# Kernel tuning notes

Measured on AMD Instinct MI355X. Metric: run time of the kernel, lower is better.

## Reference

```python
import jax, jax.numpy as jnp
import numpy as np

B, S, D, H = 2, 2048, 1024, 16
HD = D // H  # head dim = 64


def setup_inputs() -> dict:
    key0 = jax.random.key(0)
    ks = jax.random.split(key0, 12)
    scale = 1.0 / np.sqrt(D)
    inp = {
        "query": jax.random.normal(ks[0], (B, S, D), jnp.float32),
        "key": jax.random.normal(ks[1], (B, S, D), jnp.float32),
        "value": jax.random.normal(ks[2], (B, S, D), jnp.float32),
        "mask": jax.random.randint(ks[3], (B, S), 0, 2, jnp.int32),
        "Wq": jax.random.normal(ks[4], (D, D), jnp.float32) * scale,
        "bq": jnp.zeros((D,), jnp.float32),
        "Wk": jax.random.normal(ks[5], (D, D), jnp.float32) * scale,
        "bk": jnp.zeros((D,), jnp.float32),
        "Wv": jax.random.normal(ks[6], (D, D), jnp.float32) * scale,
        "bv": jnp.zeros((D,), jnp.float32),
        "Wo": jax.random.normal(ks[7], (D, D), jnp.float32) * scale,
        "bo": jnp.zeros((D,), jnp.float32),
    }
    return inp


def _split_heads(x):  # (B,S,D) -> (B,H,S,HD)
    Bb, Ss, Dd = x.shape
    return x.reshape(Bb, Ss, H, HD).transpose(0, 2, 1, 3)


def reference(query, key, value, mask, Wq, bq, Wk, bk, Wv, bv, Wo, bo):
    # Linear projections (torch Linear: x @ W.T + b), split into heads.
    q = _split_heads(query @ Wq.T + bq)
    k = _split_heads(key @ Wk.T + bk)
    v = _split_heads(value @ Wv.T + bv)
    # Scaled dot-product scores: (B,H,S,S); NOTE: original divides by sqrt(head_dim).
    scores = jnp.einsum("bhqd,bhkd->bhqk", q, k) / np.sqrt(HD).astype(np.float32)
    # mask (B,S) masks KEY positions; broadcast over heads and query positions.
    scores = jnp.where(mask[:, None, None, :] == 0, jnp.float32(-1e9), scores)
    attn = jax.nn.softmax(scores, axis=-1)
    # Dropout is identity in eval mode.
    x = jnp.einsum("bhqk,bhkd->bhqd", attn, v)  # (B,H,S,HD)
    x = x.transpose(0, 2, 1, 3).reshape(query.shape[0], query.shape[1], D)
    return x @ Wo.T + bo
```

## Files before the change

### kernel.cpp

```cpp
#include <hip/hip_runtime.h>
#include <hip/hip_bf16.h>
#include <hip/hip_fp16.h>

#define BB 2
#define SS 2048
#define DD 1024
#define HH 16
#define HD 64
#define MM (BB * SS)

typedef __attribute__((ext_vector_type(8))) _Float16 half8;
typedef __attribute__((ext_vector_type(4))) float f32x4;
typedef __attribute__((ext_vector_type(4))) short short4v;

static __device__ __forceinline__ short f2h(float f) {
    _Float16 h = (_Float16)f;
    return __builtin_bit_cast(short, h);
}

static __device__ __forceinline__ unsigned pk2(float a, float b) {
    auto h = __builtin_amdgcn_cvt_pkrtz(a, b);
    return __builtin_bit_cast(unsigned, h);
}

static __device__ __forceinline__ float fexp2(float x) {
    return __builtin_amdgcn_exp2f(x);
}

static __device__ __forceinline__ void gload16(const void* g, void* l) {
    __builtin_amdgcn_global_load_lds(
        (const __attribute__((address_space(1))) unsigned*)g,
        (__attribute__((address_space(3))) unsigned*)l, 16, 0, 0);
}

#define SC2E 0.18033688011112042f

__global__ __launch_bounds__(256) void cvt_kernel(
    const float* __restrict__ wq, const float* __restrict__ wk,
    const float* __restrict__ wv, const float* __restrict__ wo,
    const int* __restrict__ mask,
    short* __restrict__ wq16, short* __restrict__ wk16,
    short* __restrict__ wv16, short* __restrict__ wo16,
    short* __restrict__ mask16)
{
    const int i = (blockIdx.x * 256 + threadIdx.x) * 4;
    if (blockIdx.y == 4) {
        if (i >= BB * SS) return;
        const int4 mi = *(const int4*)&mask[i];
        short4v f;
        f.x = f2h(mi.x ? 1.0f : 0.0f);
        f.y = f2h(mi.y ? 1.0f : 0.0f);
        f.z = f2h(mi.z ? 1.0f : 0.0f);
        f.w = f2h(mi.w ? 1.0f : 0.0f);
        *(short4v*)&mask16[i] = f;
        return;
    }
    const float* src; short* dst;
    switch (blockIdx.y) {
        case 0: src = wq; dst = wq16; break;
        case 1: src = wk; dst = wk16; break;
        case 2: src = wv; dst = wv16; break;
        default: src = wo; dst = wo16; break;
    }
    if (i >= DD * DD) return;
    const float4 f = *(const float4*)&src[i];
    short4v h;
    h.x = f2h(f.x); h.y = f2h(f.y); h.z = f2h(f.z); h.w = f2h(f.w);
    *(short4v*)&dst[i] = h;
}

template<bool AFP32>
static __device__ __forceinline__ void gemm_phase(
    const short* __restrict__ AsCur, const short* __restrict__ BsCur,
    char* AsNxt, char* BsNxt,
    const void* __restrict__ A, const short* __restrict__ W,
    int m0, int n0, int k_next, bool do_stage,
    int t, int lr, int lq, int wc,
    f32x4 acc[4][2])
{
    constexpr int WN = 32;
    constexpr int NI = 2;
    const int K = DD;

    float4 af32[4];
    if (do_stage) {
        #pragma unroll
        for (int c = 0; c < 4; ++c) {
            const int b = c * 4096 + t * 16;
            const int row = b >> 7;
            const int coff = b & 127;
            const int scoff = coff ^ ((row & 7) << 4);
            gload16((const char*)W + ((size_t)(n0 + row) * K + k_next) * 2 + scoff,
                    BsNxt + b);
        }
        #pragma unroll
        for (int c = 0; c < 2; ++c) {
            const int b = c * 4096 + t * 16;
            const int row = b >> 7;
            const int coff = b & 127;
            if constexpr (AFP32) {
                const float* ap = (const float*)A +
                    (size_t)(m0 + row) * K + k_next + (coff >> 1);
                af32[c * 2]     = *(const float4*)ap;
                af32[c * 2 + 1] = *(const float4*)(ap + 4);
            } else {
                const int scoff = coff ^ ((row & 7) << 4);
                gload16((const char*)A + ((size_t)(m0 + row) * K + k_next) * 2 + scoff,
                        AsNxt + b);
            }
        }
    }

    half8 af[4][2], bf[NI][2];
    #pragma unroll
    for (int mi = 0; mi < 4; ++mi) {
        const int row = mi * 16 + lr;
        #pragma unroll
        for (int ks = 0; ks < 2; ++ks) {
            const int col = (ks * 32 + lq * 8) ^ ((row & 7) << 3);
            af[mi][ks] = *(const half8*)&AsCur[row * 64 + col];
        }
    }
    #pragma unroll
    for (int ni = 0; ni < NI; ++ni) {
        const int row = wc * WN + ni * 16 + lr;
        #pragma unroll
        for (int ks = 0; ks < 2; ++ks) {
            const int col = (ks * 32 + lq * 8) ^ ((row & 7) << 3);
            bf[ni][ks] = *(const half8*)&BsCur[row * 64 + col];
        }
    }
    __builtin_amdgcn_s_setprio(1);
    #pragma unroll
    for (int ks = 0; ks < 2; ++ks)
        #pragma unroll
        for (int mi = 0; mi < 4; ++mi)
            #pragma unroll
            for (int ni = 0; ni < NI; ++ni)
                acc[mi][ni] = __builtin_amdgcn_mfma_f32_16x16x32_f16(
                    af[mi][ks], bf[ni][ks], acc[mi][ni], 0, 0, 0);
    __builtin_amdgcn_s_setprio(0);

    if (do_stage) {
        if constexpr (AFP32) {
            #pragma unroll
            for (int c = 0; c < 2; ++c) {
                const int b = c * 4096 + t * 16;
                const int row = b >> 7;
                const int coff = b & 127;
                uint4 pv;
                pv.x = pk2(af32[c * 2].x,     af32[c * 2].y);
                pv.y = pk2(af32[c * 2].z,     af32[c * 2].w);
                pv.z = pk2(af32[c * 2 + 1].x, af32[c * 2 + 1].y);
                pv.w = pk2(af32[c * 2 + 1].z, af32[c * 2 + 1].w);
                *(uint4*)(AsNxt + row * 128 + (coff ^ ((row & 7) << 4))) = pv;
            }
        }
    }

    __syncthreads();
}

template<bool AFP32>
__global__ __launch_bounds__(256) void gemm_f16(
    const void* __restrict__ A0, const void* __restrict__ A1, const void* __restrict__ A2,
    const short* __restrict__ W0, const short* __restrict__ W1, const short* __restrict__ W2,
    const float* __restrict__ b0, const float* __restrict__ b1, const float* __restrict__ b2,
    void* __restrict__ C0, void* __restrict__ C1, void* __restrict__ C2,
    int mode0, int mode1, int mode2,
    float os0, float os1, float os2,
    const int* __restrict__ mask)
{
    constexpr int TM = 64;
    constexpr int WN = 32;
    constexpr int NI = 2;

    const int z = blockIdx.z;
    const void* A = (z == 0) ? A0 : (z == 1) ? A1 : A2;
    const short* W = (z == 0) ? W0 : (z == 1) ? W1 : W2;
    const float* bias = (z == 0) ? b0 : (z == 1) ? b1 : b2;
    void* C = (z == 0) ? C0 : (z == 1) ? C1 : C2;
    const int mode = (z == 0) ? mode0 : (z == 1) ? mode1 : mode2;
    const float os = (z == 0) ? os0 : (z == 1) ? os1 : os2;

    __shared__ short Asw[2][TM * 64];
    __shared__ short Bsw[2][128 * 64];

    const int t = threadIdx.x;
    const int wave = t >> 6, lane = t & 63;
    const int lr = lane & 15, lq = lane >> 4;
    const int wc = wave;
    const int m0 = blockIdx.x * TM, n0 = blockIdx.y * 128;
    const int K = DD;

    f32x4 acc[4][NI] = {};

    {
        #pragma unroll
        for (int c = 0; c < 4; ++c) {
            const int b = c * 4096 + t * 16;
            const int row = b >> 7;
            const int coff = b & 127;
            const int scoff = coff ^ ((row & 7) << 4);
            gload16((const char*)W + ((size_t)(n0 + row) * K) * 2 + scoff,
                    (char*)Bsw[0] + b);
        }
        #pragma unroll
        for (int c = 0; c < 2; ++c) {
            const int b = c * 4096 + t * 16;
            const int row = b >> 7;
            const int coff = b & 127;
            if constexpr (AFP32) {
                const float* ap = (const float*)A + (size_t)(m0 + row) * K + (coff >> 1);
                const float4 f0 = *(const float4*)ap;
                const float4 f1 = *(const float4*)(ap + 4);
                uint4 pv;
                pv.x = pk2(f0.x, f0.y);
                pv.y = pk2(f0.z, f0.w);
                pv.z = pk2(f1.x, f1.y);
                pv.w = pk2(f1.z, f1.w);
                *(uint4*)((char*)Asw[0] + row * 128 + (coff ^ ((row & 7) << 4))) = pv;
            } else {
                const int scoff = coff ^ ((row & 7) << 4);
                gload16((const char*)A + ((size_t)(m0 + row) * K) * 2 + scoff,
                        (char*)Asw[0] + b);
            }
        }
    }
    __syncthreads();

    for (int k0 = 0; k0 < K; k0 += 128) {
        gemm_phase<AFP32>(Asw[0], Bsw[0], (char*)Asw[1], (char*)Bsw[1],
                          A, W, m0, n0, k0 + 64, true,
                          t, lr, lq, wc, acc);
        gemm_phase<AFP32>(Asw[1], Bsw[1], (char*)Asw[0], (char*)Bsw[0],
                          A, W, m0, n0, k0 + 128, (k0 + 128) < K,
                          t, lr, lq, wc, acc);
    }

    if (mode == 2) {
        #pragma unroll
        for (int mi = 0; mi < 4; ++mi) {
            const int m = m0 + mi * 16 + lq * 4;
            const int bidx = m >> 11;
            const int s = m & (SS - 1);
            const int4 mk = *(const int4*)&mask[m];
            const float m0f = mk.x ? 1.0f : 0.0f;
            const float m1f = mk.y ? 1.0f : 0.0f;
            const float m2f = mk.z ? 1.0f : 0.0f;
            const float m3f = mk.w ? 1.0f : 0.0f;
            #pragma unroll
            for (int ni = 0; ni < NI; ++ni) {
                const int n = n0 + wc * WN + ni * 16 + lr;
                const int h = n >> 6, d = n & (HD - 1);
                const float bi = bias[n];
                short4v pv;
                pv.x = f2h((acc[mi][ni][0] + bi) * m0f);
                pv.y = f2h((acc[mi][ni][1] + bi) * m1f);
                pv.z = f2h((acc[mi][ni][2] + bi) * m2f);
                pv.w = f2h((acc[mi][ni][3] + bi) * m3f);
                *(short4v*)&((short*)C)[(((size_t)bidx * HH + h) * HD + d) * SS + s] = pv;
            }
        }
    } else {
        #pragma unroll
        for (int mi = 0; mi < 4; ++mi) {
            #pragma unroll
            for (int r = 0; r < 4; ++r) {
                const int m = m0 + mi * 16 + lq * 4 + r;
                const int bidx = m >> 11;
                const int s = m & (SS - 1);
                #pragma unroll
                for (int ni = 0; ni < NI; ++ni) {
                    const int n = n0 + wc * WN + ni * 16 + lr;
                    const float val = (acc[mi][ni][r] + bias[n]) * os;
                    if (mode == 0) {
                        ((float*)C)[(size_t)m * DD + n] = val;
                    } else {
                        const int h = n >> 6, d = n & (HD - 1);
                        ((short*)C)[(((size_t)bidx * HH + h) * SS + s) * HD + d] = f2h(val);
                    }
                }
            }
        }
    }
}

static __device__ __forceinline__ void attn_tile_body(
    const short* __restrict__ Ks, const short* __restrict__ Vts,
    char* KsN, char* VtsN,
    const char* kb, const char* vb,
    int kv_stage, bool do_stage,
    const short* __restrict__ mrow, int kv0,
    const half8 qf[2], short* Pw,
    int t, int lr, int lq,
    f32x4 o[4], f32x4& ol)
{
    if (do_stage) {
        #pragma unroll
        for (int c = 0; c < 2; ++c) {
            const int off = c * 4096 + t * 16;
            const int row = off >> 7, coff = off & 127;
            const int sw = coff ^ ((row & 7) << 4);
            gload16(kb + (size_t)(kv_stage + row) * 128 + sw, KsN + off);
            gload16(vb + (size_t)row * (SS * 2) + kv_stage * 2 + sw, VtsN + off);
        }
    }

    half8 mf[2];
    #pragma unroll
    for (int ks = 0; ks < 2; ++ks)
        mf[ks] = *(const half8*)&mrow[kv0 + ks * 32 + lq * 8];

    f32x4 sc[4] = {};
    __builtin_amdgcn_s_setprio(1);
    #pragma unroll
    for (int kt = 0; kt < 4; ++kt) {
        const int kr = kt * 16 + lr;
        #pragma unroll
        for (int ks = 0; ks < 2; ++ks) {
            half8 kf = *(const half8*)&Ks[kr * 64 + ((ks * 32 + lq * 8) ^ ((kr & 7) << 3))];
            sc[kt] = __builtin_amdgcn_mfma_f32_16x16x32_f16(kf, qf[ks], sc[kt], 0, 0, 0);
        }
    }
    __builtin_amdgcn_s_setprio(0);

    const int xsw = (lr & 7) << 3;
    #pragma unroll
    for (int kt = 0; kt < 4; ++kt) {
        const float p0 = fexp2(sc[kt][0]);
        const float p1 = fexp2(sc[kt][1]);
        const float p2 = fexp2(sc[kt][2]);
        const float p3 = fexp2(sc[kt][3]);
        const int cb = kt * 16 + lq * 4;
        uint2 pp;
        pp.x = pk2(p0, p1);
        pp.y = pk2(p2, p3);
        *(uint2*)&Pw[lr * 64 + (cb ^ xsw)] = pp;
    }

    half8 pf[2];
    #pragma unroll
    for (int ks = 0; ks < 2; ++ks)
        pf[ks] = *(const half8*)&Pw[lr * 64 + ((ks * 32 + lq * 8) ^ xsw)];
    __builtin_amdgcn_s_setprio(1);
    #pragma unroll
    for (int ks = 0; ks < 2; ++ks)
        ol = __builtin_amdgcn_mfma_f32_16x16x32_f16(pf[ks], mf[ks], ol, 0, 0, 0);
    #pragma unroll
    for (int dt = 0; dt < 4; ++dt) {
        const int dr = dt * 16 + lr;
        #pragma unroll
        for (int ks = 0; ks < 2; ++ks) {
            half8 vf = *(const half8*)&Vts[dr * 64 + ((ks * 32 + lq * 8) ^ ((dr & 7) << 3))];
            o[dt] = __builtin_amdgcn_mfma_f32_16x16x32_f16(pf[ks], vf, o[dt], 0, 0, 0);
        }
    }
    __builtin_amdgcn_s_setprio(0);

    __syncthreads();
}

__global__ __launch_bounds__(256) void attn_mfma_kernel(
    const short* __restrict__ q,
    const short* __restrict__ k,
    const short* __restrict__ vt,
    const short* __restrict__ mask16,
    short* __restrict__ x)
{
    const int lin = (blockIdx.z * HH + blockIdx.y) * (SS / 64) + blockIdx.x;
    const int swz = (lin & 7) * 128 + (lin >> 3);
    const int qt = swz & 31;
    const int hb = swz >> 5;
    const int h  = hb & (HH - 1);
    const int b  = hb >> 4;

    const int t = threadIdx.x;
    const int wave = t >> 6, lane = t & 63;
    const int lr = lane & 15;
    const int lq = lane >> 4;

    __shared__ short QPs[64 * 64];
    __shared__ short KsD[2][64 * 64];
    __shared__ short VtsD[2][64 * 64];

    const size_t base  = ((size_t)(b * HH + h)) * SS * HD;
    const size_t basev = ((size_t)(b * HH + h)) * HD * SS;
    const char* kb = (const char*)(k + base);
    const char* vb = (const char*)(vt + basev);

    {
        const char* qb = (const char*)(q + base + (size_t)qt * 64 * HD);
        #pragma unroll
        for (int c = 0; c < 2; ++c) {
            const int off = c * 4096 + t * 16;
            const int row = off >> 7, coff = off & 127;
            const int sw = coff ^ ((row & 7) << 4);
            gload16(qb + row * 128 + sw, (char*)QPs + off);
            gload16(kb + (size_t)row * 128 + sw, (char*)KsD[0] + off);
            gload16(vb + (size_t)row * (SS * 2) + sw, (char*)VtsD[0] + off);
        }
    }
    __syncthreads();

    half8 qf[2];
    #pragma unroll
    for (int ks = 0; ks < 2; ++ks) {
        const int r = wave * 16 + lr;
        qf[ks] = *(const half8*)&QPs[r * 64 + ((ks * 32 + lq * 8) ^ ((r & 7) << 3))];
    }
    __syncthreads();

    f32x4 o[4] = {};
    f32x4 ol = {};
    const short* mrow = &mask16[b * SS];
    short* Pw = &QPs[wave * 1024];

    for (int kv0 = 0; kv0 < SS; kv0 += 128) {
        attn_tile_body(KsD[0], VtsD[0], (char*)KsD[1], (char*)VtsD[1],
                       kb, vb, kv0 + 64, true,
                       mrow, kv0, qf, Pw, t, lr, lq, o, ol);
        attn_tile_body(KsD[1], VtsD[1], (char*)KsD[0], (char*)VtsD[0],
                       kb, vb, kv0 + 128, (kv0 + 128) < SS,
                       mrow, kv0 + 64, qf, Pw, t, lr, lq, o, ol);
    }

    float linv[4];
    #pragma unroll
    for (int r = 0; r < 4; ++r) linv[r] = 1.0f / ol[r];
    const int srow = qt * 64 + wave * 16;
    #pragma unroll
    for (int dt = 0; dt < 4; ++dt)
        #pragma unroll
        for (int r = 0; r < 4; ++r)
            x[((size_t)b * SS + srow + lq * 4 + r) * DD + h * HD + dt * 16 + lr] =
                f2h(o[dt][r] * linv[r]);
}

extern "C" void kernel_launch(void* const* d_in, const int* in_sizes, int n_in,
                              void* d_out, int out_size, void* d_ws, size_t ws_size,
                              hipStream_t stream) {
    const float* query = (const float*)d_in[0];
    const float* key   = (const float*)d_in[1];
    const float* value = (const float*)d_in[2];
    const int*   mask  = (const int*)d_in[3];
    const float* Wq = (const float*)d_in[4];
    const float* bq = (const float*)d_in[5];
    const float* Wk = (const float*)d_in[6];
    const float* bk = (const float*)d_in[7];
    const float* Wv = (const float*)d_in[8];
    const float* bv = (const float*)d_in[9];
    const float* Wo = (const float*)d_in[10];
    const float* bo = (const float*)d_in[11];
    float* out = (float*)d_out;

    const size_t NACT = (size_t)MM * DD;
    const size_t NW   = (size_t)DD * DD;
    short* wq16   = (short*)d_ws;
    short* wk16   = wq16 + NW;
    short* wv16   = wk16 + NW;
    short* wo16   = wv16 + NW;
    short* q_ws   = wo16 + NW;
    short* k_ws   = q_ws + NACT;
    short* vt_ws  = k_ws + NACT;
    short* mask16 = vt_ws + NACT;
    short* x16    = mask16 + BB * SS;

    cvt_kernel<<<dim3(NW / 4 / 256, 5), 256, 0, stream>>>(
        Wq, Wk, Wv, Wo, mask,
        wq16, wk16, wv16, wo16, mask16);

    gemm_f16<true><<<dim3(MM / 64, DD / 128, 3), 256, 0, stream>>>(
        query, key, value, wq16, wk16, wv16, bq, bk, bv,
        q_ws, k_ws, vt_ws, 1, 1, 2, SC2E, 1.0f, 1.0f, mask);

    attn_mfma_kernel<<<dim3(SS / 64, HH, BB), 256, 0, stream>>>(
        q_ws, k_ws, vt_ws, mask16, x16);

    gemm_f16<false><<<dim3(MM / 64, DD / 128, 1), 256, 0, stream>>>(
        x16, x16, x16, wo16, wo16, wo16, bo, bo, bo,
        out, out, out, 0, 0, 0, 1.0f, 1.0f, 1.0f, mask);
}
```

Measured before the change: 126.4 us.

## Triple-buffer GEMM shared tiles with explicit vmcnt waits and single barrier

Restructures the projection GEMM main loop from a double-buffered scheme with __syncthreads per phase to a three-stage ring of LDS buffers. Global-to-LDS loads for tile k+2 are issued before computing tile k, and partial s_waitcnt vmcnt counts let the barrier wait only on the older tile instead of draining all loads. For the fp32-A path, A is register-staged one tile ahead while W gets the deeper pipeline. This deepens load latency hiding at the cost of more LDS per block, which may reduce occupancy, and relies on hand-written waitcnt values being correct.

```diff
diff --git a/kernel.cpp b/kernel.cpp
--- a/kernel.cpp
+++ b/kernel.cpp
@@ -69,65 +69,83 @@
     *(short4v*)&dst[i] = h;
 }
 
-template<bool AFP32>
-static __device__ __forceinline__ void gemm_phase(
-    const short* __restrict__ AsCur, const short* __restrict__ BsCur,
-    char* AsNxt, char* BsNxt,
-    const void* __restrict__ A, const short* __restrict__ W,
-    int m0, int n0, int k_next, bool do_stage,
-    int t, int lr, int lq, int wc,
-    f32x4 acc[4][2])
-{
-    constexpr int WN = 32;
-    constexpr int NI = 2;
-    const int K = DD;
-
-    float4 af32[4];
-    if (do_stage) {
-        #pragma unroll
-        for (int c = 0; c < 4; ++c) {
-            const int b = c * 4096 + t * 16;
-            const int row = b >> 7;
-            const int coff = b & 127;
-            const int scoff = coff ^ ((row & 7) << 4);
-            gload16((const char*)W + ((size_t)(n0 + row) * K + k_next) * 2 + scoff,
-                    BsNxt + b);
-        }
-        #pragma unroll
-        for (int c = 0; c < 2; ++c) {
-            const int b = c * 4096 + t * 16;
-            const int row = b >> 7;
-            const int coff = b & 127;
-            if constexpr (AFP32) {
-                const float* ap = (const float*)A +
-                    (size_t)(m0 + row) * K + k_next + (coff >> 1);
-                af32[c * 2]     = *(const float4*)ap;
-                af32[c * 2 + 1] = *(const float4*)(ap + 4);
-            } else {
-                const int scoff = coff ^ ((row & 7) << 4);
-                gload16((const char*)A + ((size_t)(m0 + row) * K + k_next) * 2 + scoff,
-                        AsNxt + b);
-            }
-        }
-    }
-
-    half8 af[4][2], bf[NI][2];
+static __device__ __forceinline__ void stage_w(const short* W, int n0, int kk,
+                                               int t, char* dst)
+{
+    #pragma unroll
+    for (int c = 0; c < 4; ++c) {
+        const int b = c * 4096 + t * 16;
+        const int row = b >> 7;
+        const int coff = b & 127;
+        const int scoff = coff ^ ((row & 7) << 4);
+        gload16((const char*)W + ((size_t)(n0 + row) * DD + kk) * 2 + scoff, dst + b);
+    }
+}
+
+static __device__ __forceinline__ void stage_a16(const short* A, int m0, int kk,
+                                                 int t, char* dst)
+{
+    #pragma unroll
+    for (int c = 0; c < 2; ++c) {
+        const int b = c * 4096 + t * 16;
+        const int row = b >> 7;
+        const int coff = b & 127;
+        const int scoff = coff ^ ((row & 7) << 4);
+        gload16((const char*)A + ((size_t)(m0 + row) * DD + kk) * 2 + scoff, dst + b);
+    }
+}
+
+static __device__ __forceinline__ void load_a32(const float* A, int m0, int kk,
+                                                int t, float4 af32[4])
+{
+    #pragma unroll
+    for (int c = 0; c < 2; ++c) {
+        const int b = c * 4096 + t * 16;
+        const int row = b >> 7;
+        const int coff = b & 127;
+        const float* ap = A + (size_t)(m0 + row) * DD + kk + (coff >> 1);
+        af32[c * 2]     = *(const float4*)ap;
+        af32[c * 2 + 1] = *(const float4*)(ap + 4);
+    }
+}
+
+static __device__ __forceinline__ void write_a16(const float4 af32[4], int t, char* dst)
+{
+    #pragma unroll
+    for (int c = 0; c < 2; ++c) {
+        const int b = c * 4096 + t * 16;
+        const int row = b >> 7;
+        const int coff = b & 127;
+        uint4 pv;
+        pv.x = pk2(af32[c * 2].x,     af32[c * 2].y);
+        pv.y = pk2(af32[c * 2].z,     af32[c * 2].w);
+        pv.z = pk2(af32[c * 2 + 1].x, af32[c * 2 + 1].y);
+        pv.w = pk2(af32[c * 2 + 1].z, af32[c * 2 + 1].w);
+        *(uint4*)(dst + row * 128 + (coff ^ ((row & 7) << 4))) = pv;
+    }
+}
+
+static __device__ __forceinline__ void compute16(const short* As, const short* Bs,
+                                                 int lr, int lq, int wc,
+                                                 f32x4 acc[4][2])
+{
+    half8 af[4][2], bf[2][2];
     #pragma unroll
     for (int mi = 0; mi < 4; ++mi) {
         const int row = mi * 16 + lr;
         #pragma unroll
         for (int ks = 0; ks < 2; ++ks) {
             const int col = (ks * 32 + lq * 8) ^ ((row & 7) << 3);
-            af[mi][ks] = *(const half8*)&AsCur[row * 64 + col];
-        }
-    }
-    #pragma unroll
-    for (int ni = 0; ni < NI; ++ni) {
-        const int row = wc * WN + ni * 16 + lr;
+            af[mi][ks] = *(const half8*)&As[row * 64 + col];
+        }
+    }
+    #pragma unroll
+    for (int ni = 0; ni < 2; ++ni) {
+        const int row = wc * 32 + ni * 16 + lr;
         #pragma unroll
         for (int ks = 0; ks < 2; ++ks) {
             const int col = (ks * 32 + lq * 8) ^ ((row & 7) << 3);
-            bf[ni][ks] = *(const half8*)&BsCur[row * 64 + col];
+            bf[ni][ks] = *(const half8*)&Bs[row * 64 + col];
         }
     }
     __builtin_amdgcn_s_setprio(1);
@@ -136,29 +154,10 @@
         #pragma unroll
         for (int mi = 0; mi < 4; ++mi)
             #pragma unroll
-            for (int ni = 0; ni < NI; ++ni)
+            for (int ni = 0; ni < 2; ++ni)
                 acc[mi][ni] = __builtin_amdgcn_mfma_f32_16x16x32_f16(
                     af[mi][ks], bf[ni][ks], acc[mi][ni], 0, 0, 0);
     __builtin_amdgcn_s_setprio(0);
-
-    if (do_stage) {
-        if constexpr (AFP32) {
-            #pragma unroll
-            for (int c = 0; c < 2; ++c) {
-                const int b = c * 4096 + t * 16;
-                const int row = b >> 7;
-                const int coff = b & 127;
-                uint4 pv;
-                pv.x = pk2(af32[c * 2].x,     af32[c * 2].y);
-                pv.y = pk2(af32[c * 2].z,     af32[c * 2].w);
-                pv.z = pk2(af32[c * 2 + 1].x, af32[c * 2 + 1].y);
-                pv.w = pk2(af32[c * 2 + 1].z, af32[c * 2 + 1].w);
-                *(uint4*)(AsNxt + row * 128 + (coff ^ ((row & 7) << 4))) = pv;
-            }
-        }
-    }
-
-    __syncthreads();
 }
 
 template<bool AFP32>
@@ -171,8 +170,6 @@
     float os0, float os1, float os2,
     const int* __restrict__ mask)
 {
-    constexpr int TM = 64;
-    constexpr int WN = 32;
     constexpr int NI = 2;
 
     const int z = blockIdx.z;
@@ -183,59 +180,90 @@
     const int mode = (z == 0) ? mode0 : (z == 1) ? mode1 : mode2;
     const float os = (z == 0) ? os0 : (z == 1) ? os1 : os2;
 
-    __shared__ short Asw[2][TM * 64];
-    __shared__ short Bsw[2][128 * 64];
+    __shared__ short Asw[AFP32 ? 2 : 3][64 * 64];
+    __shared__ short Bsw[3][128 * 64];
 
     const int t = threadIdx.x;
     const int wave = t >> 6, lane = t & 63;
     const int lr = lane & 15, lq = lane >> 4;
     const int wc = wave;
-    const int m0 = blockIdx.x * TM, n0 = blockIdx.y * 128;
-    const int K = DD;
+    const int m0 = blockIdx.x * 64, n0 = blockIdx.y * 128;
 
     f32x4 acc[4][NI] = {};
 
-    {
-        #pragma unroll
-        for (int c = 0; c < 4; ++c) {
-            const int b = c * 4096 + t * 16;
-            const int row = b >> 7;
-            const int coff = b & 127;
-            const int scoff = coff ^ ((row & 7) << 4);
-            gload16((const char*)W + ((size_t)(n0 + row) * K) * 2 + scoff,
-                    (char*)Bsw[0] + b);
-        }
-        #pragma unroll
-        for (int c = 0; c < 2; ++c) {
-            const int b = c * 4096 + t * 16;
-            const int row = b >> 7;
-            const int coff = b & 127;
-            if constexpr (AFP32) {
-                const float* ap = (const float*)A + (size_t)(m0 + row) * K + (coff >> 1);
-                const float4 f0 = *(const float4*)ap;
-                const float4 f1 = *(const float4*)(ap + 4);
-                uint4 pv;
-                pv.x = pk2(f0.x, f0.y);
-                pv.y = pk2(f0.z, f0.w);
-                pv.z = pk2(f1.x, f1.y);
-                pv.w = pk2(f1.z, f1.w);
-                *(uint4*)((char*)Asw[0] + row * 128 + (coff ^ ((row & 7) << 4))) = pv;
-            } else {
-                const int scoff = coff ^ ((row & 7) << 4);
-                gload16((const char*)A + ((size_t)(m0 + row) * K) * 2 + scoff,
-                        (char*)Asw[0] + b);
-            }
-        }
-    }
-    __syncthreads();
-
-    for (int k0 = 0; k0 < K; k0 += 128) {
-        gemm_phase<AFP32>(Asw[0], Bsw[0], (char*)Asw[1], (char*)Bsw[1],
-                          A, W, m0, n0, k0 + 64, true,
-                          t, lr, lq, wc, acc);
-        gemm_phase<AFP32>(Asw[1], Bsw[1], (char*)Asw[0], (char*)Bsw[0],
-                          A, W, m0, n0, k0 + 128, (k0 + 128) < K,
-                          t, lr, lq, wc, acc);
+    short* w0p = (short*)Bsw[0];
+    short* w1p = (short*)Bsw[1];
+    short* w2p = (short*)Bsw[2];
+
+    if constexpr (AFP32) {
+        short* aC = (short*)Asw[0];
+        short* aN = (short*)Asw[1];
+        float4 af32[4];
+
+        load_a32((const float*)A, m0, 0, t, af32);
+        __builtin_amdgcn_sched_barrier(0);
+        stage_w(W, n0, 0, t, (char*)w0p);
+        stage_w(W, n0, 64, t, (char*)w1p);
+        write_a16(af32, t, (char*)aC);
+        asm volatile("s_waitcnt vmcnt(4) lgkmcnt(0)" ::: "memory");
+        __builtin_amdgcn_s_barrier();
+        asm volatile("" ::: "memory");
+
+        for (int j = 0; j < 14; ++j) {
+            load_a32((const float*)A, m0, (j + 1) * 64, t, af32);
+            __builtin_amdgcn_sched_barrier(0);
+            stage_w(W, n0, (j + 2) * 64, t, (char*)w2p);
+            compute16(aC, w0p, lr, lq, wc, acc);
+            write_a16(af32, t, (char*)aN);
+            asm volatile("s_waitcnt lgkmcnt(0)" ::: "memory");
+            __builtin_amdgcn_s_barrier();
+            asm volatile("" ::: "memory");
+            short* ta = aC; aC = aN; aN = ta;
+            short* tw = w0p; w0p = w1p; w1p = w2p; w2p = tw;
+        }
+        load_a32((const float*)A, m0, 15 * 64, t, af32);
+        compute16(aC, w0p, lr, lq, wc, acc);
+        write_a16(af32, t, (char*)aN);
+        asm volatile("s_waitcnt lgkmcnt(0)" ::: "memory");
+        __builtin_amdgcn_s_barrier();
+        asm volatile("" ::: "memory");
+        {
+            short* ta = aC; aC = aN; aN = ta;
+            short* tw = w0p; w0p = w1p; w1p = w2p; w2p = tw;
+        }
+        compute16(aC, w0p, lr, lq, wc, acc);
+    } else {
+        short* a0p = (short*)Asw[0];
+        short* a1p = (short*)Asw[1];
+        short* a2p = (short*)Asw[2];
+
+        stage_a16((const short*)A, m0, 0, t, (char*)a0p);
+        stage_w(W, n0, 0, t, (char*)w0p);
+        stage_a16((const short*)A, m0, 64, t, (char*)a1p);
+        stage_w(W, n0, 64, t, (char*)w1p);
+        asm volatile("s_waitcnt vmcnt(6)" ::: "memory");
+        __builtin_amdgcn_s_barrier();
+        asm volatile("" ::: "memory");
+
+        for (int j = 0; j < 14; ++j) {
+            stage_a16((const short*)A, m0, (j + 2) * 64, t, (char*)a2p);
+            stage_w(W, n0, (j + 2) * 64, t, (char*)w2p);
+            compute16(a0p, w0p, lr, lq, wc, acc);
+            asm volatile("s_waitcnt vmcnt(6)" ::: "memory");
+            __builtin_amdgcn_s_barrier();
+            asm volatile("" ::: "memory");
+            short* ta = a0p; a0p = a1p; a1p = a2p; a2p = ta;
+            short* tw = w0p; w0p = w1p; w1p = w2p; w2p = tw;
+        }
+        compute16(a0p, w0p, lr, lq, wc, acc);
+        asm volatile("s_waitcnt vmcnt(0)" ::: "memory");
+        __builtin_amdgcn_s_barrier();
+        asm volatile("" ::: "memory");
+        {
+            short* ta = a0p; a0p = a1p; a1p = a2p; a2p = ta;
+            short* tw = w0p; w0p = w1p; w1p = w2p; w2p = tw;
+        }
+        compute16(a0p, w0p, lr, lq, wc, acc);
     }
 
     if (mode == 2) {
@@ -251,7 +279,7 @@
             const float m3f = mk.w ? 1.0f : 0.0f;
             #pragma unroll
             for (int ni = 0; ni < NI; ++ni) {
-                const int n = n0 + wc * WN + ni * 16 + lr;
+                const int n = n0 + wc * 32 + ni * 16 + lr;
                 const int h = n >> 6, d = n & (HD - 1);
                 const float bi = bias[n];
                 short4v pv;
@@ -272,7 +300,7 @@
                 const int s = m & (SS - 1);
                 #pragma unroll
                 for (int ni = 0; ni < NI; ++ni) {
-                    const int n = n0 + wc * WN + ni * 16 + lr;
+                    const int n = n0 + wc * 32 + ni * 16 + lr;
                     const float val = (acc[mi][ni][r] + bias[n]) * os;
                     if (mode == 0) {
                         ((float*)C)[(size_t)m * DD + n] = val;
```

Result: slower. 129.6 us (+2.5%).
